# Performance work log

Hardware: AMD Instinct MI355X
Metric: run time of the kernel (lower is better)

## Reference

```python
import jax, jax.numpy as jnp
import numpy as np
from jax import lax

B = 65536

def _conv(x, w, b):
    y = lax.conv_general_dilated(x, w, (1, 1), 'VALID',
                                 dimension_numbers=('NCHW', 'OIHW', 'NCHW'))
    return y + b[None, :, None, None]

def _maxpool2(x):
    return lax.reduce_window(x, -jnp.inf, lax.max, (1, 1, 2, 2), (1, 1, 2, 2), 'VALID')

def _cnot01(s):  # control wire0, target wire1; s: [B,2,2] indexed [b,q0,q1]
    return jnp.stack([s[:, 0, :], s[:, 1, ::-1]], axis=1)

def _cnot10(s):  # control wire1, target wire0
    return jnp.stack([s[:, :, 0], s[:, ::-1, 1]], axis=2)

def _ry(half_angle):  # RY(2*half_angle) as used in circuit (theta/2 = half_angle)
    c, si = jnp.cos(half_angle), jnp.sin(half_angle)
    return jnp.stack([jnp.stack([c, -si]), jnp.stack([si, c])]).astype(jnp.complex64)

def _apply_w0(s, U):
    return jnp.einsum('ij,bjk->bik', U, s)

def _apply_w1(s, U):
    return jnp.einsum('ij,bkj->bki', U, s)

def _quantum(x2, p):
    # x2: [B,2] float32, p: [8] float32. Batched 2-qubit statevector sim.
    x0, x1 = x2[:, 0], x2[:, 1]
    n = x2.shape[0]
    s = jnp.full((n, 2, 2), 0.5 + 0.0j, dtype=jnp.complex64)  # H|0> x H|0>
    # RZ(2*x0) on wire 0: diag(e^{-i x0}, e^{i x0})
    s = s * jnp.exp(1j * jnp.stack([-x0, x0], axis=1).astype(jnp.complex64))[:, :, None]
    # RZ(2*x1) on wire 1
    s = s * jnp.exp(1j * jnp.stack([-x1, x1], axis=1).astype(jnp.complex64))[:, None, :]
    s = _cnot01(s)
    ang = (jnp.pi - x0) * (jnp.pi - x1)  # RZ(2*ang) on wire 1
    s = s * jnp.exp(1j * jnp.stack([-ang, ang], axis=1).astype(jnp.complex64))[:, None, :]
    s = _cnot01(s)
    s = _apply_w0(s, _ry(p[0])); s = _apply_w1(s, _ry(p[1])); s = _cnot01(s)
    s = _apply_w0(s, _ry(p[2])); s = _apply_w1(s, _ry(p[3])); s = _cnot10(s)
    s = _apply_w0(s, _ry(p[4])); s = _apply_w1(s, _ry(p[5])); s = _cnot01(s)
    s = _apply_w0(s, _ry(p[6])); s = _apply_w1(s, _ry(p[7]))
    z = jnp.array([[1.0, -1.0], [-1.0, 1.0]], dtype=jnp.float32)  # Z0 (x) Z1 signs
    prob = (s.real ** 2 + s.imag ** 2)
    return jnp.sum(prob * z[None], axis=(1, 2))  # [B]

def setup_inputs() -> dict:
    key = jax.random.key(0)
    ks = jax.random.split(key, 12)
    d = {}
    d['x'] = jax.random.normal(ks[0], (B, 1, 28, 28), dtype=jnp.float32)
    d['conv1_w'] = jax.random.normal(ks[1], (2, 1, 5, 5), dtype=jnp.float32) * 0.2
    d['conv1_b'] = jax.random.normal(ks[2], (2,), dtype=jnp.float32) * 0.1
    d['conv2_w'] = jax.random.normal(ks[3], (16, 2, 5, 5), dtype=jnp.float32) * 0.14
    d['conv2_b'] = jax.random.normal(ks[4], (16,), dtype=jnp.float32) * 0.1
    d['fc1_w'] = jax.random.normal(ks[5], (64, 256), dtype=jnp.float32) * 0.0625
    d['fc1_b'] = jax.random.normal(ks[6], (64,), dtype=jnp.float32) * 0.05
    d['fc2_w'] = jax.random.normal(ks[7], (2, 64), dtype=jnp.float32) * 0.125
    d['fc2_b'] = jax.random.normal(ks[8], (2,), dtype=jnp.float32) * 0.05
    d['fc3_w'] = jax.random.normal(ks[9], (1, 1), dtype=jnp.float32)
    d['fc3_b'] = jax.random.normal(ks[10], (1,), dtype=jnp.float32) * 0.05
    d['qnn_params'] = jax.random.uniform(ks[11], (8,), dtype=jnp.float32)
    return d

def reference(x, conv1_w, conv1_b, conv2_w, conv2_b, fc1_w, fc1_b,
              fc2_w, fc2_b, fc3_w, fc3_b, qnn_params):
    h = jax.nn.relu(_conv(x, conv1_w, conv1_b))        # [B,2,24,24]
    h = _maxpool2(h)                                    # [B,2,12,12]
    h = jax.nn.relu(_conv(h, conv2_w, conv2_b))        # [B,16,8,8]
    h = _maxpool2(h)                                    # [B,16,4,4]
    # Dropout2d: identity in eval mode
    h = h.reshape(h.shape[0], -1)                       # [B,256]
    h = jax.nn.relu(h @ fc1_w.T + fc1_b)                # [B,64]
    h = h @ fc2_w.T + fc2_b                             # [B,2]
    q = _quantum(h, qnn_params)[:, None]                # [B,1]
    y = q @ fc3_w.T + fc3_b                             # [B,1]
    logits = jnp.concatenate([y, 1.0 - y], axis=-1)     # [B,2]
    return jax.nn.log_softmax(logits, axis=1)
```

## Files before the change

kernel.cpp:

```cpp
#include <hip/hip_runtime.h>
#include <math.h>


typedef float v2f __attribute__((ext_vector_type(2)));
typedef float f32x4 __attribute__((ext_vector_type(4)));
typedef short bf16x8 __attribute__((ext_vector_type(8)));
typedef unsigned int u32x4 __attribute__((ext_vector_type(4)));

union B8 { unsigned int u[4]; bf16x8 v; };

static __device__ __forceinline__ v2f vmax2(v2f a, v2f b) {
    return __builtin_elementwise_max(a, b);
}

#define PK_FMA_W0(acc, w, xp) \
    asm("v_pk_fma_f32 %0, %1, %2, %0 op_sel:[0,0,0] op_sel_hi:[1,0,1]" \
        : "+v"(acc) : "s"(w), "v"(xp))
#define PK_FMA_W1(acc, w, xp) \
    asm("v_pk_fma_f32 %0, %1, %2, %0 op_sel:[0,1,0] op_sel_hi:[1,1,1]" \
        : "+v"(acc) : "s"(w), "v"(xp))

#define MFMA16(a, b, c) __builtin_amdgcn_mfma_f32_16x16x32_bf16(a, b, c, 0, 0, 0)

#define SEL_HI 0x07060302u
#define SEL_LO 0x05040100u

static __device__ __forceinline__ unsigned int pack1(float v) {
    unsigned int hi = __float_as_uint(v) & 0xFFFF0000u;
    float lo = v - __uint_as_float(hi);
    return hi | (__float_as_uint(lo) >> 16);
}

#define A2_HI 0
#define A2_LO 1536
#define A1_HI 3072
#define A1_LO (3072 + 16384)

#define P1_S 296
#define HB_S 260

__global__ __launch_bounds__(256)
void hqcnn_prep(const float* __restrict__ w2, const float* __restrict__ fw1,
                unsigned short* __restrict__ ws) {
    int t = blockIdx.x * 256 + threadIdx.x;
    if (blockIdx.x == 0) {
        for (int e = threadIdx.x; e < 1536; e += 256) {
            int cc = e >> 9, r = e & 511;
            int m = r >> 5, kl = r & 31;
            int q = kl >> 3, j = kl & 7;
            int row = cc * 4 + q;
            int ch = (row >= 5) ? 1 : 0;
            int u = row - 5 * ch;
            float val = (row < 10 && j < 5) ? w2[m * 50 + ch * 25 + u * 5 + j] : 0.f;
            unsigned int uu = __float_as_uint(val);
            float lo = val - __uint_as_float(uu & 0xFFFF0000u);
            ws[A2_HI + e] = (unsigned short)(uu >> 16);
            ws[A2_LO + e] = (unsigned short)(__float_as_uint(lo) >> 16);
        }
    }
    for (int e = t; e < 16384; e += gridDim.x * 256) {
        float val = fw1[e];
        unsigned int u = __float_as_uint(val);
        float lo = val - __uint_as_float(u & 0xFFFF0000u);
        ws[A1_HI + e] = (unsigned short)(u >> 16);
        ws[A1_LO + e] = (unsigned short)(__float_as_uint(lo) >> 16);
    }
}

__global__ __launch_bounds__(256, 6)
void hqcnn_fused(const float* __restrict__ x,
                 const float* __restrict__ w1,
                 const float* __restrict__ b1,
                 const float* __restrict__ b2,
                 const float* __restrict__ fb1,
                 const float* __restrict__ fw2,
                 const float* __restrict__ fb2,
                 const float* __restrict__ fw3,
                 const float* __restrict__ fb3,
                 const float* __restrict__ qp,
                 const unsigned short* __restrict__ ws,
                 float* __restrict__ out)
{
    __shared__ __align__(16) unsigned int p1u[8 * P1_S];
    __shared__ __align__(16) unsigned int hbu[8 * HB_S];
    __shared__ __align__(16) float zbuf[4 * 32];

    const int t = threadIdx.x;
    const int wv = t >> 6;
    const int lane = t & 63;
    const int n = lane & 15;
    const int q = lane >> 4;
    const long base = (long)blockIdx.x * 8;

    if (lane < 16)
        p1u[(2 * wv + (lane >> 3)) * P1_S + 288 + (lane & 7)] = 0u;

    {
        v2f w1p[25];
        #pragma unroll
        for (int k = 0; k < 25; ++k)
            w1p[k] = (v2f){w1[k], w1[25 + k]};
        const v2f bias1 = (v2f){b1[0], b1[1]};

        #pragma unroll
        for (int it = 0; it < 2; ++it) {
            int f = lane + it * 64;
            if (f < 96) {
                int s = f / 48;
                int r = f - s * 48;
                int i = r >> 2, jh = r & 3;
                const float* xrow = x + (base + 2 * wv + s) * 784;
                v2f acc[12];
                #pragma unroll
                for (int qq = 0; qq < 12; ++qq) acc[qq] = (v2f){0.f, 0.f};
                #pragma unroll
                for (int u = 0; u < 6; ++u) {
                    const v2f* xp = (const v2f*)(xrow + (2 * i + u) * 28 + 6 * jh);
                    v2f P[5] = { xp[0], xp[1], xp[2], xp[3], xp[4] };
                    #pragma unroll
                    for (int a = 0; a < 2; ++a) {
                        if (a <= u && (u - a) <= 4) {
                            const int wu = u - a;
                            #pragma unroll
                            for (int v = 0; v < 5; ++v) {
                                #pragma unroll
                                for (int j = 0; j < 6; ++j) {
                                    const int e = j + v;
                                    if (e & 1) { PK_FMA_W1(acc[a * 6 + j], w1p[wu * 5 + v], P[e >> 1]); }
                                    else       { PK_FMA_W0(acc[a * 6 + j], w1p[wu * 5 + v], P[e >> 1]); }
                                }
                            }
                        }
                    }
                }
                #pragma unroll
                for (int m = 0; m < 3; ++m) {
                    v2f mx = vmax2(vmax2(acc[2 * m], acc[2 * m + 1]),
                                   vmax2(acc[6 + 2 * m], acc[7 + 2 * m]));
                    mx = mx + bias1;
                    mx = vmax2(mx, (v2f){0.f, 0.f});
                    int pc = 3 * jh + m;
                    int off = (2 * wv + s) * P1_S + i * 12 + pc;
                    p1u[off] = pack1(mx.x);
                    p1u[off + 144] = pack1(mx.y);
                }
            }
        }
    }
    asm volatile("s_waitcnt lgkmcnt(0)" ::: "memory");

    {
        const bf16x8* A2h = (const bf16x8*)(ws + A2_HI);
        const bf16x8* A2l = (const bf16x8*)(ws + A2_LO);
        bf16x8 a_h[3], a_l[3];
        #pragma unroll
        for (int cc = 0; cc < 3; ++cc) {
            a_h[cc] = A2h[cc * 64 + n * 4 + q];
            a_l[cc] = A2l[cc * 64 + n * 4 + q];
        }
        int chu[3];
        #pragma unroll
        for (int cc = 0; cc < 3; ++cc) {
            int row = cc * 4 + q;
            int ch = (row >= 5) ? 1 : 0;
            int u = row - 5 * ch;
            chu[cc] = (row < 10) ? (ch * 144 + u * 12) : -1;
        }
        f32x4 bias4 = *(const f32x4*)(b2 + q * 4);

        for (int t8 = 0; t8 < 8; ++t8) {
            int smp = 2 * wv + (t8 >> 2);
            int tt = t8 & 3;
            int prow = 2 * tt + (n >> 3);
            int pcol = n & 7;
            int pbase = smp * P1_S + prow * 12 + pcol;
            int zaddr = smp * P1_S + 288;
            f32x4 acc = {0.f, 0.f, 0.f, 0.f};
            f32x4 acc2 = {0.f, 0.f, 0.f, 0.f};
            #pragma unroll
            for (int cc = 0; cc < 3; ++cc) {
                int a = (chu[cc] >= 0) ? (pbase + chu[cc]) : zaddr;
                unsigned int e0 = p1u[a],     e1 = p1u[a + 1], e2 = p1u[a + 2],
                             e3 = p1u[a + 3], e4 = p1u[a + 4];
                B8 BH, BL;
                BH.u[0] = __builtin_amdgcn_perm(e1, e0, SEL_HI);
                BH.u[1] = __builtin_amdgcn_perm(e3, e2, SEL_HI);
                BH.u[2] = e4 >> 16;
                BH.u[3] = 0u;
                BL.u[0] = __builtin_amdgcn_perm(e1, e0, SEL_LO);
                BL.u[1] = __builtin_amdgcn_perm(e3, e2, SEL_LO);
                BL.u[2] = e4 & 0xFFFFu;
                BL.u[3] = 0u;
                acc  = MFMA16(a_h[cc], BH.v, acc);
                acc2 = MFMA16(a_h[cc], BL.v, acc2);
                acc  = MFMA16(a_l[cc], BH.v, acc);
            }
            acc = acc + acc2;
            #pragma unroll
            for (int r = 0; r < 4; ++r) {
                float vmx = acc[r];
                vmx = fmaxf(vmx, __shfl_xor(vmx, 1, 64));
                vmx = fmaxf(vmx, __shfl_xor(vmx, 8, 64));
                float pv = fmaxf(vmx + bias4[r], 0.f);
                if ((n & 1) == 0 && n < 8) {
                    int jc = n >> 1;
                    hbu[smp * HB_S + (q * 4 + r) * 16 + tt * 4 + jc] = pack1(pv);
                }
            }
        }
    }
    __syncthreads();

    {
        const bf16x8* A1h = (const bf16x8*)(ws + A1_HI);
        const bf16x8* A1l = (const bf16x8*)(ws + A1_LO);
        const int abase = (wv * 16 + n) * 32 + q;
        f32x4 acc = {0.f, 0.f, 0.f, 0.f};
        f32x4 acc2 = {0.f, 0.f, 0.f, 0.f};
        #pragma unroll
        for (int kk = 0; kk < 8; ++kk) {
            bf16x8 ah = A1h[abase + kk * 4];
            bf16x8 al = A1l[abase + kk * 4];
            B8 BH, BL;
            if (n < 8) {
                const u32x4* hp = (const u32x4*)(hbu + n * HB_S + kk * 32 + q * 8);
                u32x4 d0 = hp[0], d1 = hp[1];
                BH.u[0] = __builtin_amdgcn_perm(d0.y, d0.x, SEL_HI);
                BH.u[1] = __builtin_amdgcn_perm(d0.w, d0.z, SEL_HI);
                BH.u[2] = __builtin_amdgcn_perm(d1.y, d1.x, SEL_HI);
                BH.u[3] = __builtin_amdgcn_perm(d1.w, d1.z, SEL_HI);
                BL.u[0] = __builtin_amdgcn_perm(d0.y, d0.x, SEL_LO);
                BL.u[1] = __builtin_amdgcn_perm(d0.w, d0.z, SEL_LO);
                BL.u[2] = __builtin_amdgcn_perm(d1.y, d1.x, SEL_LO);
                BL.u[3] = __builtin_amdgcn_perm(d1.w, d1.z, SEL_LO);
            } else {
                BH.u[0] = BH.u[1] = BH.u[2] = BH.u[3] = 0u;
                BL.u[0] = BL.u[1] = BL.u[2] = BL.u[3] = 0u;
            }
            acc  = MFMA16(ah, BH.v, acc);
            acc2 = MFMA16(ah, BL.v, acc2);
            acc  = MFMA16(al, BH.v, acc);
        }
        acc = acc + acc2;
        f32x4 fb4 = *(const f32x4*)(fb1 + wv * 16 + q * 4);
        f32x4 w20 = *(const f32x4*)(fw2 + wv * 16 + q * 4);
        f32x4 w21 = *(const f32x4*)(fw2 + 64 + wv * 16 + q * 4);
        float p0 = 0.f, p1v = 0.f;
        #pragma unroll
        for (int r = 0; r < 4; ++r) {
            float a = fmaxf(acc[r] + fb4[r], 0.f);
            p0  = fmaf(a, w20[r], p0);
            p1v = fmaf(a, w21[r], p1v);
        }
        p0  += __shfl_xor(p0, 16, 64);  p0  += __shfl_xor(p0, 32, 64);
        p1v += __shfl_xor(p1v, 16, 64); p1v += __shfl_xor(p1v, 32, 64);
        if (q == 0) {
            zbuf[wv * 32 + n * 2]     = p0;
            zbuf[wv * 32 + n * 2 + 1] = p1v;
        }
    }
    __syncthreads();

    {
        int s = t & 7;
        float x0 = fb2[0] + zbuf[s * 2]     + zbuf[32 + s * 2]
                          + zbuf[64 + s * 2] + zbuf[96 + s * 2];
        float x1 = fb2[1] + zbuf[s * 2 + 1] + zbuf[32 + s * 2 + 1]
                          + zbuf[64 + s * 2 + 1] + zbuf[96 + s * 2 + 1];

        float sr[4], si[4];
        {
            float th0 = -x0 - x1, th1 = -x0 + x1, th2 = x0 - x1, th3 = x0 + x1;
            sr[0] = 0.5f * __cosf(th0); si[0] = 0.5f * __sinf(th0);
            sr[1] = 0.5f * __cosf(th1); si[1] = 0.5f * __sinf(th1);
            sr[2] = 0.5f * __cosf(th2); si[2] = 0.5f * __sinf(th2);
            sr[3] = 0.5f * __cosf(th3); si[3] = 0.5f * __sinf(th3);
        }
        {
            float tr = sr[2]; sr[2] = sr[3]; sr[3] = tr;
            float ti = si[2]; si[2] = si[3]; si[3] = ti;
            float ang = ((float)M_PI - x0) * ((float)M_PI - x1);
            float ca = __cosf(ang), sa = __sinf(ang);
            float r, im;
            r = sr[0]; im = si[0]; sr[0] = r*ca + im*sa; si[0] = im*ca - r*sa;
            r = sr[2]; im = si[2]; sr[2] = r*ca + im*sa; si[2] = im*ca - r*sa;
            r = sr[1]; im = si[1]; sr[1] = r*ca - im*sa; si[1] = im*ca + r*sa;
            r = sr[3]; im = si[3]; sr[3] = r*ca - im*sa; si[3] = im*ca + r*sa;
            tr = sr[2]; sr[2] = sr[3]; sr[3] = tr;
            ti = si[2]; si[2] = si[3]; si[3] = ti;
        }
        float cp[8], sp[8];
        #pragma unroll
        for (int g = 0; g < 8; ++g) { float qv = qp[g]; cp[g] = __cosf(qv); sp[g] = __sinf(qv); }

        #define QRY0(cc, ss) { \
            float a0r=sr[0], a0i=si[0], a1r=sr[2], a1i=si[2]; \
            sr[0]=cc*a0r-ss*a1r; si[0]=cc*a0i-ss*a1i; \
            sr[2]=ss*a0r+cc*a1r; si[2]=ss*a0i+cc*a1i; \
            float b0r=sr[1], b0i=si[1], b1r=sr[3], b1i=si[3]; \
            sr[1]=cc*b0r-ss*b1r; si[1]=cc*b0i-ss*b1i; \
            sr[3]=ss*b0r+cc*b1r; si[3]=ss*b0i+cc*b1i; }
        #define QRY1(cc, ss) { \
            float a0r=sr[0], a0i=si[0], a1r=sr[1], a1i=si[1]; \
            sr[0]=cc*a0r-ss*a1r; si[0]=cc*a0i-ss*a1i; \
            sr[1]=ss*a0r+cc*a1r; si[1]=ss*a0i+cc*a1i; \
            float b0r=sr[2], b0i=si[2], b1r=sr[3], b1i=si[3]; \
            sr[2]=cc*b0r-ss*b1r; si[2]=cc*b0i-ss*b1i; \
            sr[3]=ss*b0r+cc*b1r; si[3]=ss*b0i+cc*b1i; }
        #define QSWAP(i_, j_) { float tr=sr[i_]; sr[i_]=sr[j_]; sr[j_]=tr; \
                                float ti=si[i_]; si[i_]=si[j_]; si[j_]=ti; }

        QRY0(cp[0], sp[0]);
        QRY1(cp[1], sp[1]);
        QSWAP(2, 3);
        QRY0(cp[2], sp[2]);
        QRY1(cp[3], sp[3]);
        QSWAP(1, 3);
        QRY0(cp[4], sp[4]);
        QRY1(cp[5], sp[5]);
        QSWAP(2, 3);
        QRY0(cp[6], sp[6]);
        QRY1(cp[7], sp[7]);

        float qv = (sr[0]*sr[0] + si[0]*si[0])
                 - (sr[1]*sr[1] + si[1]*si[1])
                 - (sr[2]*sr[2] + si[2]*si[2])
                 + (sr[3]*sr[3] + si[3]*si[3]);
        float y = fmaf(qv, fw3[0], fb3[0]);
        float l0 = y, l1 = 1.0f - y;
        float m = fmaxf(l0, l1);
        float lse = m + __logf(__expf(l0 - m) + __expf(l1 - m));
        if (t < 16) {
            int comp = t >> 3;
            out[(base + s) * 2 + comp] = comp ? (l1 - lse) : (l0 - lse);
        }
        #undef QRY0
        #undef QRY1
        #undef QSWAP
    }
}

extern "C" void kernel_launch(void* const* d_in, const int* in_sizes, int n_in,
                              void* d_out, int out_size, void* d_ws, size_t ws_size,
                              hipStream_t stream) {
    const float* x   = (const float*)d_in[0];
    const float* w1  = (const float*)d_in[1];
    const float* b1  = (const float*)d_in[2];
    const float* w2  = (const float*)d_in[3];
    const float* b2  = (const float*)d_in[4];
    const float* fw1 = (const float*)d_in[5];
    const float* fb1 = (const float*)d_in[6];
    const float* fw2 = (const float*)d_in[7];
    const float* fb2 = (const float*)d_in[8];
    const float* fw3 = (const float*)d_in[9];
    const float* fb3 = (const float*)d_in[10];
    const float* qp  = (const float*)d_in[11];
    float* outp = (float*)d_out;
    unsigned short* wsp = (unsigned short*)d_ws;

    hipLaunchKernelGGL(hqcnn_prep, dim3(64), dim3(256), 0, stream, w2, fw1, wsp);

    int B = in_sizes[0] / 784;
    int nblk = B / 8;
    hipLaunchKernelGGL(hqcnn_fused, dim3(nblk), dim3(256), 0, stream,
                       x, w1, b1, b2, fb1, fw2, fb2, fw3, fb3, qp, wsp, outp);
}
```

Before: 402.1 us.

## Swap MFMA operand roles in conv2 to pool in-register and spread conv1 across block

The conv2 MFMA now uses patches as the A operand and weights as B, with output pixels arranged so each lane's four accumulator rows form a 2x2 pool window. This replaces the cross-lane shuffles and predicated stores with an in-register max and one store per lane. The fc1 weight prepack is permuted to match the new hbu layout. Conv1 work is redistributed across all 256 threads with a block barrier instead of a per-wave wait, which adds a sync but balances the load.

```diff
diff --git a/kernel.cpp b/kernel.cpp
--- a/kernel.cpp
+++ b/kernel.cpp
@@ -46,12 +46,12 @@
     if (blockIdx.x == 0) {
         for (int e = threadIdx.x; e < 1536; e += 256) {
             int cc = e >> 9, r = e & 511;
-            int m = r >> 5, kl = r & 31;
-            int q = kl >> 3, j = kl & 7;
-            int row = cc * 4 + q;
+            int lid = r >> 3, j = r & 7;
+            int nn = lid & 15, qq = lid >> 4;
+            int row = cc * 4 + qq;
             int ch = (row >= 5) ? 1 : 0;
             int u = row - 5 * ch;
-            float val = (row < 10 && j < 5) ? w2[m * 50 + ch * 25 + u * 5 + j] : 0.f;
+            float val = (row < 10 && j < 5) ? w2[nn * 50 + ch * 25 + u * 5 + j] : 0.f;
             unsigned int uu = __float_as_uint(val);
             float lo = val - __uint_as_float(uu & 0xFFFF0000u);
             ws[A2_HI + e] = (unsigned short)(uu >> 16);
@@ -59,7 +59,9 @@
         }
     }
     for (int e = t; e < 16384; e += gridDim.x * 256) {
-        float val = fw1[e];
+        int m = e >> 8, kp = e & 255;
+        int oc = kp & 15, s16 = kp >> 4;
+        float val = fw1[m * 256 + oc * 16 + s16];
         unsigned int u = __float_as_uint(val);
         float lo = val - __uint_as_float(u & 0xFFFF0000u);
         ws[A1_HI + e] = (unsigned short)(u >> 16);
@@ -92,8 +94,8 @@
     const int q = lane >> 4;
     const long base = (long)blockIdx.x * 8;
 
-    if (lane < 16)
-        p1u[(2 * wv + (lane >> 3)) * P1_S + 288 + (lane & 7)] = 0u;
+    if (t < 64)
+        p1u[(t >> 3) * P1_S + 288 + (t & 7)] = 0u;
 
     {
         v2f w1p[25];
@@ -104,12 +106,12 @@
 
         #pragma unroll
         for (int it = 0; it < 2; ++it) {
-            int f = lane + it * 64;
-            if (f < 96) {
+            int f = t + it * 256;
+            if (f < 384) {
                 int s = f / 48;
                 int r = f - s * 48;
                 int i = r >> 2, jh = r & 3;
-                const float* xrow = x + (base + 2 * wv + s) * 784;
+                const float* xrow = x + (base + s) * 784;
                 v2f acc[12];
                 #pragma unroll
                 for (int qq = 0; qq < 12; ++qq) acc[qq] = (v2f){0.f, 0.f};
@@ -140,24 +142,28 @@
                     mx = mx + bias1;
                     mx = vmax2(mx, (v2f){0.f, 0.f});
                     int pc = 3 * jh + m;
-                    int off = (2 * wv + s) * P1_S + i * 12 + pc;
+                    int off = s * P1_S + i * 12 + pc;
                     p1u[off] = pack1(mx.x);
                     p1u[off + 144] = pack1(mx.y);
                 }
             }
         }
     }
-    asm volatile("s_waitcnt lgkmcnt(0)" ::: "memory");
+    __syncthreads();
 
     {
-        const bf16x8* A2h = (const bf16x8*)(ws + A2_HI);
-        const bf16x8* A2l = (const bf16x8*)(ws + A2_LO);
-        bf16x8 a_h[3], a_l[3];
+        const bf16x8* B2h = (const bf16x8*)(ws + A2_HI);
+        const bf16x8* B2l = (const bf16x8*)(ws + A2_LO);
+        bf16x8 b_h[3], b_l[3];
         #pragma unroll
         for (int cc = 0; cc < 3; ++cc) {
-            a_h[cc] = A2h[cc * 64 + n * 4 + q];
-            a_l[cc] = A2l[cc * 64 + n * 4 + q];
-        }
+            b_h[cc] = B2h[cc * 64 + lane];
+            b_l[cc] = B2l[cc * 64 + lane];
+        }
+        const int quad = n >> 2;
+        const int di = (n >> 1) & 1;
+        const int dj = n & 1;
+        const int scol = 2 * quad + dj;
         int chu[3];
         #pragma unroll
         for (int cc = 0; cc < 3; ++cc) {
@@ -166,14 +172,13 @@
             int u = row - 5 * ch;
             chu[cc] = (row < 10) ? (ch * 144 + u * 12) : -1;
         }
-        f32x4 bias4 = *(const f32x4*)(b2 + q * 4);
-
+        const float bias = b2[n];
+
+        #pragma unroll 2
         for (int t8 = 0; t8 < 8; ++t8) {
             int smp = 2 * wv + (t8 >> 2);
             int tt = t8 & 3;
-            int prow = 2 * tt + (n >> 3);
-            int pcol = n & 7;
-            int pbase = smp * P1_S + prow * 12 + pcol;
+            int pbase = smp * P1_S + (2 * tt + di) * 12 + scol;
             int zaddr = smp * P1_S + 288;
             f32x4 acc = {0.f, 0.f, 0.f, 0.f};
             f32x4 acc2 = {0.f, 0.f, 0.f, 0.f};
@@ -182,31 +187,23 @@
                 int a = (chu[cc] >= 0) ? (pbase + chu[cc]) : zaddr;
                 unsigned int e0 = p1u[a],     e1 = p1u[a + 1], e2 = p1u[a + 2],
                              e3 = p1u[a + 3], e4 = p1u[a + 4];
-                B8 BH, BL;
-                BH.u[0] = __builtin_amdgcn_perm(e1, e0, SEL_HI);
-                BH.u[1] = __builtin_amdgcn_perm(e3, e2, SEL_HI);
-                BH.u[2] = e4 >> 16;
-                BH.u[3] = 0u;
-                BL.u[0] = __builtin_amdgcn_perm(e1, e0, SEL_LO);
-                BL.u[1] = __builtin_amdgcn_perm(e3, e2, SEL_LO);
-                BL.u[2] = e4 & 0xFFFFu;
-                BL.u[3] = 0u;
-                acc  = MFMA16(a_h[cc], BH.v, acc);
-                acc2 = MFMA16(a_h[cc], BL.v, acc2);
-                acc  = MFMA16(a_l[cc], BH.v, acc);
+                B8 AH, AL;
+                AH.u[0] = __builtin_amdgcn_perm(e1, e0, SEL_HI);
+                AH.u[1] = __builtin_amdgcn_perm(e3, e2, SEL_HI);
+                AH.u[2] = e4 >> 16;
+                AH.u[3] = 0u;
+                AL.u[0] = __builtin_amdgcn_perm(e1, e0, SEL_LO);
+                AL.u[1] = __builtin_amdgcn_perm(e3, e2, SEL_LO);
+                AL.u[2] = e4 & 0xFFFFu;
+                AL.u[3] = 0u;
+                acc  = MFMA16(AH.v, b_h[cc], acc);
+                acc2 = MFMA16(AL.v, b_h[cc], acc2);
+                acc  = MFMA16(AH.v, b_l[cc], acc);
             }
             acc = acc + acc2;
-            #pragma unroll
-            for (int r = 0; r < 4; ++r) {
-                float vmx = acc[r];
-                vmx = fmaxf(vmx, __shfl_xor(vmx, 1, 64));
-                vmx = fmaxf(vmx, __shfl_xor(vmx, 8, 64));
-                float pv = fmaxf(vmx + bias4[r], 0.f);
-                if ((n & 1) == 0 && n < 8) {
-                    int jc = n >> 1;
-                    hbu[smp * HB_S + (q * 4 + r) * 16 + tt * 4 + jc] = pack1(pv);
-                }
-            }
+            float pv = fmaxf(fmaxf(acc[0], acc[1]), fmaxf(acc[2], acc[3]));
+            pv = fmaxf(pv + bias, 0.f);
+            hbu[smp * HB_S + (tt * 4 + q) * 16 + n] = pack1(pv);
         }
     }
     __syncthreads();
```

Result: faster. 385.9 us (-4.0%).
